# Optimization experiments

Hardware: AMD Instinct MI355X
Metric: run time of the kernel (lower is better)

## Reference

```python
import math
import jax, jax.numpy as jnp
import numpy as np

B, S, H = 2, 2048, 1024
NH = 16
HD = H // NH            # 64
ROT = int(HD * 0.25)    # 16
QKV_SLOTS = 1024
PROJ_SLOTS = 1024
FFN_SLOTS = 4096
EPS = 1e-5


def gelu_l2_norm(x, axis=-1):
    # F.gelu (exact erf) then L2-normalize and rescale by sqrt(dim)
    g = jax.nn.gelu(x, approximate=False)
    n = jnp.linalg.norm(g, ord=2, axis=axis, keepdims=True)
    return g / n * math.sqrt(g.shape[axis])


def layer_norm(x, w, b):
    mu = jnp.mean(x, axis=-1, keepdims=True)
    var = jnp.mean(jnp.square(x - mu), axis=-1, keepdims=True)
    return (x - mu) * jax.lax.rsqrt(var + EPS) * w + b


def pattention(x, key_tok, val_tok):
    # [.., in] @ [slots, in]^T -> [.., slots]; NOTE: scale MULTIPLIES (as in source)
    aw = jnp.einsum('bsh,ph->bsp', x, key_tok) * math.sqrt(x.shape[-1])
    aw = gelu_l2_norm(aw, axis=-1)
    return jnp.einsum('bsp,pd->bsd', aw, val_tok)


def rotary_cos_sin(seq_len, rot_dim, base=10000.0):
    inv_freq = 1.0 / (base ** (jnp.arange(0, rot_dim, 2, dtype=jnp.float32) / rot_dim))
    t = jnp.arange(seq_len, dtype=jnp.float32)
    freqs = jnp.einsum('s,d->sd', t, inv_freq)           # [S, rot/2]
    emb = jnp.concatenate([freqs, freqs], axis=-1)       # [S, rot]
    return jnp.cos(emb), jnp.sin(emb)


def rotate_half(x):
    x1, x2 = jnp.split(x, 2, axis=-1)
    return jnp.concatenate([-x2, x1], axis=-1)


def setup_inputs() -> dict:
    key = jax.random.key(0)
    ks = jax.random.split(key, 12)
    p = lambda k, shape: jax.random.normal(k, shape, dtype=jnp.float32) * 0.02
    return {
        'x': jax.random.normal(ks[0], (B, S, H), dtype=jnp.float32),
        'ln1_w': jnp.ones((H,), jnp.float32), 'ln1_b': jnp.zeros((H,), jnp.float32),
        'ln2_w': jnp.ones((H,), jnp.float32), 'ln2_b': jnp.zeros((H,), jnp.float32),
        'q_key': p(ks[1], (QKV_SLOTS, H)), 'q_val': p(ks[2], (QKV_SLOTS, H)),
        'k_key': p(ks[3], (QKV_SLOTS, H)), 'k_val': p(ks[4], (QKV_SLOTS, H)),
        'v_key': p(ks[5], (QKV_SLOTS, H)), 'v_val': p(ks[6], (QKV_SLOTS, H)),
        'proj_key': p(ks[7], (PROJ_SLOTS, H)), 'proj_val': p(ks[8], (PROJ_SLOTS, H)),
        'ffn_key': p(ks[9], (FFN_SLOTS, H)), 'ffn_val': p(ks[10], (FFN_SLOTS, H)),
    }


def reference(x, ln1_w, ln1_b, ln2_w, ln2_b, q_key, q_val, k_key, k_val,
              v_key, v_val, proj_key, proj_val, ffn_key, ffn_val):
    residual = x
    xn = layer_norm(x, ln1_w, ln1_b)
    q = pattention(xn, q_key, q_val).reshape(B, S, NH, HD)
    k = pattention(xn, k_key, k_val).reshape(B, S, NH, HD)
    v = pattention(xn, v_key, v_val).reshape(B, S, NH, HD)

    cos, sin = rotary_cos_sin(S, ROT)          # [S, ROT]
    cos = cos[None, :, None, :]
    sin = sin[None, :, None, :]
    q_rot, q_pass = q[..., :ROT], q[..., ROT:]
    k_rot, k_pass = k[..., :ROT], k[..., ROT:]
    q_rot = q_rot * cos + rotate_half(q_rot) * sin
    k_rot = k_rot * cos + rotate_half(k_rot) * sin
    q = jnp.concatenate([q_rot, q_pass], axis=-1).transpose(0, 2, 1, 3)  # [B,NH,S,HD]
    k = jnp.concatenate([k_rot, k_pass], axis=-1).transpose(0, 2, 1, 3)
    v = v.transpose(0, 2, 1, 3)

    scale = math.sqrt(HD)
    causal = jnp.triu(jnp.ones((S, S), dtype=bool), k=1)
    attn_mask = jnp.where(causal, jnp.float32(-10000.0), jnp.float32(0.0))
    aw = jnp.einsum('bhqd,bhkd->bhqk', q, k) / scale + attn_mask
    aw = gelu_l2_norm(aw, axis=-1)
    o = jnp.einsum('bhqk,bhkd->bhqd', aw, v)
    o = o.transpose(0, 2, 1, 3).reshape(B, S, H)

    x = residual + pattention(o, proj_key, proj_val)
    residual = x
    x = residual + pattention(layer_norm(x, ln2_w, ln2_b), ffn_key, ffn_val)
    return x
```

## Files before the change

### kernel.cpp

```cpp
#include <hip/hip_runtime.h>

typedef __bf16 bf16x8 __attribute__((ext_vector_type(8)));
typedef float f32x4 __attribute__((ext_vector_type(4)));
typedef unsigned short u16;

__device__ __forceinline__ float b2f(u16 u) {
  union { unsigned int i; float f; } v; v.i = ((unsigned int)u) << 16; return v.f;
}
__device__ __forceinline__ u16 f2b(float f) {
  union { float f; unsigned int i; } v; v.f = f;
  unsigned int x = v.i;
  x += 0x7fffu + ((x >> 16) & 1u);
  return (u16)(x >> 16);
}
__device__ __forceinline__ float gelu_f(float x) {
  float x2 = x * x;
  float p = x * (1.5957691216f + 0.0713548162f * x2);
  float e = __expf(p);
  float r = __builtin_amdgcn_rcpf(1.0f + e);
  return x - x * r;
}
__device__ __forceinline__ void async16(const u16* g, u16* l) {
  __builtin_amdgcn_global_load_lds(
      (const __attribute__((address_space(1))) void*)g,
      (__attribute__((address_space(3))) void*)l, 16, 0, 0);
}
__device__ __forceinline__ void swz(int& bn, int& bm, int& bz) {
  int gx = (int)gridDim.x, gy = (int)gridDim.y;
  int flat = (int)(blockIdx.x + gridDim.x * (blockIdx.y + gridDim.y * blockIdx.z));
  int seq = flat >> 3;
  int nbm = gy >> 3;
  bm = (flat & 7) * nbm + seq % nbm;
  int rest = seq / nbm;
  bn = rest % gx;
  bz = rest / gx;
}

union U4 { uint4 u; u16 s[8]; };
union PF { bf16x8 v; u16 s[8]; };

__global__ __launch_bounds__(256) void cvt9_kernel(
    const float* __restrict__ qk, const float* __restrict__ kk,
    const float* __restrict__ vk, const float* __restrict__ pk,
    const float* __restrict__ fk, u16* __restrict__ w, float* __restrict__ ssqz) {
  int z = blockIdx.y;
  int i = blockIdx.x * 256 + threadIdx.x;
  if (z == 8) {
    if (i < 20480) ssqz[i] = 0.f;
    return;
  }
  const float* in = (z == 0) ? qk : (z == 1) ? kk : (z == 2) ? vk : (z == 3) ? pk
                    : fk + (size_t)(z - 4) * 1048576;
  u16* o = w + (size_t)z * 1048576;
  float4 f = ((const float4*)in)[i];
  ushort4 s;
  s.x = f2b(f.x); s.y = f2b(f.y); s.z = f2b(f.z); s.w = f2b(f.w);
  ((ushort4*)o)[i] = s;
}

__global__ __launch_bounds__(256) void cvtT8_kernel(
    const float* __restrict__ qv, const float* __restrict__ kv,
    const float* __restrict__ vv, const float* __restrict__ pv,
    const float* __restrict__ fv, u16* __restrict__ valsT, u16* __restrict__ fvT) {
  __shared__ float t[32][33];
  int z = blockIdx.z;
  const float* in; u16* o; int Rout, rowoff;
  if (z < 4) {
    in = (z == 0) ? qv : (z == 1) ? kv : (z == 2) ? vv : pv;
    o = valsT + (size_t)z * 1048576; Rout = 1024; rowoff = 0;
  } else {
    in = fv + (size_t)(z - 4) * 1048576;
    o = fvT; Rout = 4096; rowoff = (z - 4) * 1024;
  }
  int bc = blockIdx.x, br = blockIdx.y;
  int tid = threadIdx.x;
  int r = tid >> 5, cc = tid & 31;
  #pragma unroll
  for (int i = 0; i < 4; ++i)
    t[r + i * 8][cc] = in[(size_t)(br * 32 + r + i * 8) * 1024 + bc * 32 + cc];
  __syncthreads();
  #pragma unroll
  for (int i = 0; i < 4; ++i)
    o[(size_t)(bc * 32 + r + i * 8) * Rout + rowoff + br * 32 + cc] = f2b(t[cc][r + i * 8]);
}

__global__ __launch_bounds__(256) void ln_kernel(const float* __restrict__ x,
    const float* __restrict__ w, const float* __restrict__ b, u16* __restrict__ out) {
  int wv = threadIdx.x >> 6, lane = threadIdx.x & 63;
  int row = blockIdx.x * 4 + wv;
  const float* xr = x + (size_t)row * 1024;
  float4 v[4];
  float s = 0.f, s2 = 0.f;
  #pragma unroll
  for (int i = 0; i < 4; ++i) {
    v[i] = ((const float4*)xr)[lane + 64 * i];
    s += v[i].x + v[i].y + v[i].z + v[i].w;
    s2 += v[i].x * v[i].x + v[i].y * v[i].y + v[i].z * v[i].z + v[i].w * v[i].w;
  }
  #pragma unroll
  for (int m = 1; m < 64; m <<= 1) { s += __shfl_xor(s, m); s2 += __shfl_xor(s2, m); }
  float mu = s * (1.0f / 1024.0f);
  float inv = rsqrtf(s2 * (1.0f / 1024.0f) - mu * mu + 1e-5f);
  u16* orow = out + (size_t)row * 1024;
  #pragma unroll
  for (int i = 0; i < 4; ++i) {
    int c = (lane + 64 * i) * 4;
    ushort4 o;
    o.x = f2b((v[i].x - mu) * inv * w[c]     + b[c]);
    o.y = f2b((v[i].y - mu) * inv * w[c + 1] + b[c + 1]);
    o.z = f2b((v[i].z - mu) * inv * w[c + 2] + b[c + 2]);
    o.w = f2b((v[i].w - mu) * inv * w[c + 3] + b[c + 3]);
    ((ushort4*)orow)[lane + 64 * i] = o;
  }
}

__device__ __forceinline__ bf16x8 ldfrag(const u16* __restrict__ base, int row, int ks, int quad) {
  int off = (row * 64 + ks * 32 + quad * 8) ^ ((row & 7) << 3);
  return *(const bf16x8*)&base[off];
}

template <int EPI, bool ROT>
__global__ __launch_bounds__(512, 2) void gemm8(
    const u16* __restrict__ A, size_t sAz,
    const u16* __restrict__ B, size_t sBz,
    u16* __restrict__ C, size_t sCz,
    float* __restrict__ ssqb, size_t sSz,
    int N, int K, float alpha) {
  __shared__ __align__(16) u16 As[2][2][8192];
  __shared__ __align__(16) u16 Bs[2][2][8192];
  int bn, bm, bz;
  swz(bn, bm, bz);
  int tid = threadIdx.x, lane = tid & 63, wv = tid >> 6;
  int quad = lane >> 4, l16 = lane & 15;
  int wm = wv >> 2, wn = wv & 3;
  const u16* Ab = A + (size_t)bz * sAz + (size_t)(bm * 256) * K;
  const u16* Bb = B + (size_t)bz * sBz + (size_t)(bn * 256) * K;
  size_t off0, off1;
  {
    int r0 = wv * 16 + (lane >> 3);
    int r1 = r0 + 8;
    off0 = (size_t)r0 * K + ((lane & 7) ^ (r0 & 7)) * 8;
    off1 = (size_t)r1 * K + ((lane & 7) ^ (r1 & 7)) * 8;
  }
  int lds0 = wv * 1024, lds1 = wv * 1024 + 512;
  const size_t hK = (size_t)128 * K;
  auto STAGE = [&](const u16* gb, int k0, u16* lds) {
    async16(gb + off0 + k0, lds + lds0);
    async16(gb + off1 + k0, lds + lds1);
  };

  f32x4 zero = {0.f, 0.f, 0.f, 0.f};
  f32x4 acc[8][4];
  #pragma unroll
  for (int i = 0; i < 8; ++i)
    #pragma unroll
    for (int j = 0; j < 4; ++j) acc[i][j] = zero;

  int NT = K >> 6;
  STAGE(Bb,      0, &Bs[0][0][0]);
  STAGE(Bb + hK, 0, &Bs[0][1][0]);
  STAGE(Ab,      0, &As[0][0][0]);
  STAGE(Ab + hK, 0, &As[0][1][0]);
  STAGE(Bb,      64, &Bs[1][0][0]);
  STAGE(Bb + hK, 64, &Bs[1][1][0]);
  STAGE(Ab,      64, &As[1][0][0]);
  asm volatile("s_waitcnt vmcnt(6)" ::: "memory");
  __builtin_amdgcn_sched_barrier(0);
  __builtin_amdgcn_s_barrier();

  bf16x8 a[4][2], b[4][2];
  int brow = (wn & 1) * 64;
  for (int t = 0; t < NT; ++t) {
    int cur = t & 1;
    const u16* Ar = &As[cur][wm][0];
    const u16* Br = &Bs[cur][wn >> 1][0];
    #pragma unroll
    for (int j = 0; j < 4; ++j)
      #pragma unroll
      for (int ks = 0; ks < 2; ++ks)
        b[j][ks] = ldfrag(Br, brow + j * 16 + l16, ks, quad);
    #pragma unroll
    for (int i = 0; i < 4; ++i)
      #pragma unroll
      for (int ks = 0; ks < 2; ++ks)
        a[i][ks] = ldfrag(Ar, i * 16 + l16, ks, quad);
    if (t + 1 < NT) STAGE(Ab + hK, (t + 1) * 64, &As[cur ^ 1][1][0]);
    __builtin_amdgcn_s_barrier();
    asm volatile("s_waitcnt lgkmcnt(0)" ::: "memory");
    __builtin_amdgcn_sched_barrier(0);
    __builtin_amdgcn_s_setprio(1);
    #pragma unroll
    for (int i = 0; i < 4; ++i)
      #pragma unroll
      for (int j = 0; j < 2; ++j) {
        acc[i][j] = __builtin_amdgcn_mfma_f32_16x16x32_bf16(a[i][0], b[j][0], acc[i][j], 0, 0, 0);
        acc[i][j] = __builtin_amdgcn_mfma_f32_16x16x32_bf16(a[i][1], b[j][1], acc[i][j], 0, 0, 0);
      }
    __builtin_amdgcn_s_setprio(0);
    __builtin_amdgcn_sched_barrier(0);
    __builtin_amdgcn_s_barrier();
    if (t + 2 < NT) STAGE(Bb, (t + 2) * 64, &Bs[cur][0][0]);
    __builtin_amdgcn_s_barrier();
    __builtin_amdgcn_s_setprio(1);
    #pragma unroll
    for (int i = 0; i < 4; ++i)
      #pragma unroll
      for (int j = 2; j < 4; ++j) {
        acc[i][j] = __builtin_amdgcn_mfma_f32_16x16x32_bf16(a[i][0], b[j][0], acc[i][j], 0, 0, 0);
        acc[i][j] = __builtin_amdgcn_mfma_f32_16x16x32_bf16(a[i][1], b[j][1], acc[i][j], 0, 0, 0);
      }
    __builtin_amdgcn_s_setprio(0);
    __builtin_amdgcn_sched_barrier(0);
    __builtin_amdgcn_s_barrier();
    #pragma unroll
    for (int i = 0; i < 4; ++i)
      #pragma unroll
      for (int ks = 0; ks < 2; ++ks)
        a[i][ks] = ldfrag(Ar, 64 + i * 16 + l16, ks, quad);
    if (t + 2 < NT) STAGE(Bb + hK, (t + 2) * 64, &Bs[cur][1][0]);
    __builtin_amdgcn_s_barrier();
    asm volatile("s_waitcnt lgkmcnt(0)" ::: "memory");
    __builtin_amdgcn_sched_barrier(0);
    __builtin_amdgcn_s_setprio(1);
    #pragma unroll
    for (int i = 0; i < 4; ++i)
      #pragma unroll
      for (int j = 0; j < 2; ++j) {
        acc[4 + i][j] = __builtin_amdgcn_mfma_f32_16x16x32_bf16(a[i][0], b[j][0], acc[4 + i][j], 0, 0, 0);
        acc[4 + i][j] = __builtin_amdgcn_mfma_f32_16x16x32_bf16(a[i][1], b[j][1], acc[4 + i][j], 0, 0, 0);
      }
    __builtin_amdgcn_s_setprio(0);
    __builtin_amdgcn_sched_barrier(0);
    __builtin_amdgcn_s_barrier();
    if (t + 2 < NT) STAGE(Ab, (t + 2) * 64, &As[cur][0][0]);
    __builtin_amdgcn_s_barrier();
    __builtin_amdgcn_s_setprio(1);
    #pragma unroll
    for (int i = 0; i < 4; ++i)
      #pragma unroll
      for (int j = 2; j < 4; ++j) {
        acc[4 + i][j] = __builtin_amdgcn_mfma_f32_16x16x32_bf16(a[i][0], b[j][0], acc[4 + i][j], 0, 0, 0);
        acc[4 + i][j] = __builtin_amdgcn_mfma_f32_16x16x32_bf16(a[i][1], b[j][1], acc[4 + i][j], 0, 0, 0);
      }
    __builtin_amdgcn_s_setprio(0);
    if (t < NT - 1) {
      if (t == NT - 2) asm volatile("s_waitcnt vmcnt(0)" ::: "memory");
      else             asm volatile("s_waitcnt vmcnt(6)" ::: "memory");
    }
    __builtin_amdgcn_sched_barrier(0);
    __builtin_amdgcn_s_barrier();
  }

  #pragma unroll
  for (int i = 0; i < 8; ++i) {
    int rbase = bm * 256 + wm * 128 + i * 16 + quad * 4;
    if (EPI == 0) {
      float srow[4] = {0.f, 0.f, 0.f, 0.f};
      #pragma unroll
      for (int j = 0; j < 4; ++j) {
        int c = bn * 256 + wn * 64 + j * 16 + l16;
        #pragma unroll
        for (int reg = 0; reg < 4; ++reg) {
          float g = gelu_f(acc[i][j][reg] * alpha);
          srow[reg] += g * g;
          C[(size_t)bz * sCz + (size_t)(rbase + reg) * N + c] = f2b(g);
        }
      }
      #pragma unroll
      for (int reg = 0; reg < 4; ++reg) {
        float s = srow[reg];
        s += __shfl_xor(s, 1); s += __shfl_xor(s, 2);
        s += __shfl_xor(s, 4); s += __shfl_xor(s, 8);
        if (l16 == 0) atomicAdd(&ssqb[bz * sSz + rbase + reg], s);
      }
    } else {
      float sc[4];
      #pragma unroll
      for (int reg = 0; reg < 4; ++reg)
        sc[reg] = alpha * rsqrtf(ssqb[bz * sSz + rbase + reg]);
      #pragma unroll
      for (int j = 0; j < 4; ++j) {
        int c = bn * 256 + wn * 64 + j * 16 + l16;
        #pragma unroll
        for (int reg = 0; reg < 4; ++reg) {
          float vs = acc[i][j][reg] * sc[reg];
          if (ROT && j == 0) {
            float prt = __shfl_xor(vs, 8);
            if (bz < 2) {
              int seq = (rbase + reg) & 2047;
              float fr = exp2f((float)(l16 & 7) * -1.66096404744368f);
              float ang = (float)seq * fr;
              float c_ = __cosf(ang), s_ = __sinf(ang);
              vs = (l16 < 8) ? (vs * c_ - prt * s_) : (vs * c_ + prt * s_);
            }
          }
          C[(size_t)bz * sCz + (size_t)(rbase + reg) * N + c] = f2b(vs);
        }
      }
    }
  }
}

template <int TM>
__global__ __launch_bounds__(256) void gemm_key(
    const u16* __restrict__ A, size_t sAz,
    const u16* __restrict__ B, size_t sBz,
    u16* __restrict__ C, size_t sCz,
    float* __restrict__ ssqb, size_t sSz,
    int N, int K, float alpha) {
  constexpr int AI = TM / 32;
  __shared__ __align__(16) u16 As[2][TM * 32];
  __shared__ __align__(16) u16 Bs[2][128 * 32];
  int bn, bm, bz;
  swz(bn, bm, bz);
  const u16* Ab = A + (size_t)bz * sAz + (size_t)bm * TM * K;
  const u16* Bb = B + (size_t)bz * sBz + (size_t)bn * 128 * K;
  int tid = threadIdx.x, lane = tid & 63, wv = tid >> 6;
  int quad = lane >> 4, l16 = lane & 15;
  int lr = lane >> 2, lc = (lane & 3) * 8;
  int wm = wv >> 1, wn = wv & 1;
  int RB = wm * (TM / 2), CB = wn * 64;
  f32x4 zero = {0.f, 0.f, 0.f, 0.f};
  f32x4 acc[AI][4];
  #pragma unroll
  for (int i = 0; i < AI; ++i)
    #pragma unroll
    for (int j = 0; j < 4; ++j) acc[i][j] = zero;
  #pragma unroll
  for (int t = 0; t < TM / 64; ++t) {
    int ia = wv * (TM / 64) + t;
    async16(Ab + (size_t)(ia * 16 + lr) * K + lc, &As[0][ia * 512]);
  }
  #pragma unroll
  for (int t = 0; t < 2; ++t) {
    int ib = wv * 2 + t;
    async16(Bb + (size_t)(ib * 16 + lr) * K + lc, &Bs[0][ib * 512]);
  }
  for (int k0 = 0, cur = 0; k0 < K; k0 += 32, cur ^= 1) {
    __syncthreads();
    if (k0 + 32 < K) {
      #pragma unroll
      for (int t = 0; t < TM / 64; ++t) {
        int ia = wv * (TM / 64) + t;
        async16(Ab + (size_t)(ia * 16 + lr) * K + k0 + 32 + lc, &As[cur ^ 1][ia * 512]);
      }
      #pragma unroll
      for (int t = 0; t < 2; ++t) {
        int ib = wv * 2 + t;
        async16(Bb + (size_t)(ib * 16 + lr) * K + k0 + 32 + lc, &Bs[cur ^ 1][ib * 512]);
      }
    }
    bf16x8 af[AI], bf[4];
    #pragma unroll
    for (int i = 0; i < AI; ++i)
      af[i] = *(const bf16x8*)&As[cur][(RB + i * 16 + l16) * 32 + quad * 8];
    #pragma unroll
    for (int j = 0; j < 4; ++j)
      bf[j] = *(const bf16x8*)&Bs[cur][(CB + j * 16 + l16) * 32 + quad * 8];
    #pragma unroll
    for (int i = 0; i < AI; ++i)
      #pragma unroll
      for (int j = 0; j < 4; ++j)
        acc[i][j] = __builtin_amdgcn_mfma_f32_16x16x32_bf16(af[i], bf[j], acc[i][j], 0, 0, 0);
  }
  #pragma unroll
  for (int i = 0; i < AI; ++i) {
    int rbase = bm * TM + RB + i * 16 + quad * 4;
    float srow[4] = {0.f, 0.f, 0.f, 0.f};
    #pragma unroll
    for (int j = 0; j < 4; ++j) {
      int c = bn * 128 + CB + j * 16 + l16;
      #pragma unroll
      for (int reg = 0; reg < 4; ++reg) {
        float g = gelu_f(acc[i][j][reg] * alpha);
        srow[reg] += g * g;
        C[(size_t)bz * sCz + (size_t)(rbase + reg) * N + c] = f2b(g);
      }
    }
    #pragma unroll
    for (int reg = 0; reg < 4; ++reg) {
      float s = srow[reg];
      s += __shfl_xor(s, 1); s += __shfl_xor(s, 2);
      s += __shfl_xor(s, 4); s += __shfl_xor(s, 8);
      if (l16 == 0) atomicAdd(&ssqb[bz * sSz + rbase + reg], s);
    }
  }
}

template <int TM, int MODE, bool ROT>
__global__ __launch_bounds__(256) void gemm_val(
    const u16* __restrict__ A, size_t sAz,
    const u16* __restrict__ B, size_t sBz,
    void* __restrict__ C, size_t sCz,
    const float* __restrict__ ssqb, size_t sSz,
    int N, int K, int kzs, int klen, float sqrtP, const float* __restrict__ res) {
  constexpr int AI = TM / 32;
  __shared__ __align__(16) u16 As[2][TM * 32];
  __shared__ __align__(16) u16 Bs[2][128 * 32];
  int bn, bm, bz;
  swz(bn, bm, bz);
  const u16* Ab = A + (size_t)bz * sAz + (size_t)bm * TM * K;
  const u16* Bb = B + (size_t)bz * sBz + (size_t)bn * 128 * K;
  int tid = threadIdx.x, lane = tid & 63, wv = tid >> 6;
  int quad = lane >> 4, l16 = lane & 15;
  int lr = lane >> 2, lc = (lane & 3) * 8;
  int wm = wv >> 1, wn = wv & 1;
  int RB = wm * (TM / 2), CB = wn * 64;
  f32x4 zero = {0.f, 0.f, 0.f, 0.f};
  f32x4 acc[AI][4];
  #pragma unroll
  for (int i = 0; i < AI; ++i)
    #pragma unroll
    for (int j = 0; j < 4; ++j) acc[i][j] = zero;
  int kb0 = bz * kzs;
  #pragma unroll
  for (int t = 0; t < TM / 64; ++t) {
    int ia = wv * (TM / 64) + t;
    async16(Ab + (size_t)(ia * 16 + lr) * K + kb0 + lc, &As[0][ia * 512]);
  }
  #pragma unroll
  for (int t = 0; t < 2; ++t) {
    int ib = wv * 2 + t;
    async16(Bb + (size_t)(ib * 16 + lr) * K + kb0 + lc, &Bs[0][ib * 512]);
  }
  for (int k0 = kb0, cur = 0; k0 < kb0 + klen; k0 += 32, cur ^= 1) {
    __syncthreads();
    if (k0 + 32 < kb0 + klen) {
      #pragma unroll
      for (int t = 0; t < TM / 64; ++t) {
        int ia = wv * (TM / 64) + t;
        async16(Ab + (size_t)(ia * 16 + lr) * K + k0 + 32 + lc, &As[cur ^ 1][ia * 512]);
      }
      #pragma unroll
      for (int t = 0; t < 2; ++t) {
        int ib = wv * 2 + t;
        async16(Bb + (size_t)(ib * 16 + lr) * K + k0 + 32 + lc, &Bs[cur ^ 1][ib * 512]);
      }
    }
    bf16x8 af[AI], bf[4];
    #pragma unroll
    for (int i = 0; i < AI; ++i)
      af[i] = *(const bf16x8*)&As[cur][(RB + i * 16 + l16) * 32 + quad * 8];
    #pragma unroll
    for (int j = 0; j < 4; ++j)
      bf[j] = *(const bf16x8*)&Bs[cur][(CB + j * 16 + l16) * 32 + quad * 8];
    #pragma unroll
    for (int i = 0; i < AI; ++i)
      #pragma unroll
      for (int j = 0; j < 4; ++j)
        acc[i][j] = __builtin_amdgcn_mfma_f32_16x16x32_bf16(af[i], bf[j], acc[i][j], 0, 0, 0);
  }
  #pragma unroll
  for (int i = 0; i < AI; ++i) {
    int rbase = bm * TM + RB + i * 16 + quad * 4;
    float sc[4];
    if (MODE < 2) {
      #pragma unroll
      for (int reg = 0; reg < 4; ++reg)
        sc[reg] = sqrtP * rsqrtf(ssqb[bz * sSz + rbase + reg]);
    }
    #pragma unroll
    for (int j = 0; j < 4; ++j) {
      int c = bn * 128 + CB + j * 16 + l16;
      #pragma unroll
      for (int reg = 0; reg < 4; ++reg) {
        float v = acc[i][j][reg];
        size_t idx = (size_t)(rbase + reg) * N + c;
        if (MODE == 0) {
          float vs = v * sc[reg];
          if (ROT && j == 0) {
            float prt = __shfl_xor(vs, 8);
            if (bz < 2) {
              int seq = (rbase + reg) & 2047;
              float fr = exp2f((float)(l16 & 7) * -1.66096404744368f);
              float ang = (float)seq * fr;
              float c_ = __cosf(ang), s_ = __sinf(ang);
              vs = (l16 < 8) ? (vs * c_ - prt * s_) : (vs * c_ + prt * s_);
            }
          }
          ((u16*)C)[(size_t)bz * sCz + idx] = f2b(vs);
        } else if (MODE == 1) {
          ((float*)C)[idx] = v * sc[reg] + res[idx];
        } else {
          ((float*)C)[(size_t)bz * sCz + idx] = v;
        }
      }
    }
  }
}

__global__ __launch_bounds__(256) void vt_kernel(const u16* __restrict__ vb,
                                                 u16* __restrict__ vT) {
  __shared__ __align__(16) u16 T[64][72];
  int st = blockIdx.x, bh = blockIdx.y;
  int b = bh >> 4, h = bh & 15;
  int tid = threadIdx.x;
  #pragma unroll
  for (int i = 0; i < 2; ++i) {
    int l = tid + 256 * i;
    int s = l >> 3, dc = l & 7;
    *(uint4*)&T[s][dc * 8] =
        *(const uint4*)(vb + (size_t)(b * 2048 + st * 64 + s) * 1024 + h * 64 + dc * 8);
  }
  __syncthreads();
  #pragma unroll
  for (int i = 0; i < 2; ++i) {
    int l = tid + 256 * i;
    int d = l >> 3, scid = l & 7;
    int blk = (scid >> 2) * 32;
    int qq = (scid & 3) * 4;
    U4 u;
    #pragma unroll
    for (int j = 0; j < 8; ++j)
      u.s[j] = T[blk + (j >> 2) * 16 + qq + (j & 3)][d];
    *(uint4*)(vT + ((size_t)bh * 64 + d) * 2048 + st * 64 + scid * 8) = u.u;
  }
}

__global__ __launch_bounds__(256) void attn_kernel(
    const u16* __restrict__ qb, const u16* __restrict__ kb,
    const u16* __restrict__ vT, u16* __restrict__ ob) {
  __shared__ __align__(16) u16 Qs[64 * 64];
  __shared__ __align__(16) u16 Ks[2][64 * 64];
  __shared__ __align__(16) u16 Vts[2][64 * 64];
  int bh = blockIdx.x;
  int qt = 31 - (int)blockIdx.y;
  int b = bh >> 4, h = bh & 15;
  const u16* qp = qb + (size_t)b * 2048 * 1024 + h * 64;
  const u16* kp = kb + (size_t)b * 2048 * 1024 + h * 64;
  const u16* vp = vT + (size_t)bh * 64 * 2048;
  int tid = threadIdx.x, lane = tid & 63, wv = tid >> 6;
  int quad = lane >> 4, l16 = lane & 15;
  int lr8 = lane >> 3, lc8 = (lane & 7) * 8;
  int MR = wv * 16;
  int nkt = qt + 1;
  #pragma unroll
  for (int t = 0; t < 2; ++t) {
    int idx = wv * 2 + t;
    async16(qp + (size_t)(qt * 64 + idx * 8 + lr8) * 1024 + lc8, &Qs[idx * 512]);
    async16(kp + (size_t)(idx * 8 + lr8) * 1024 + lc8, &Ks[0][idx * 512]);
    async16(vp + (size_t)(idx * 8 + lr8) * 2048 + lc8, &Vts[0][idx * 512]);
  }
  f32x4 zero = {0.f, 0.f, 0.f, 0.f};
  f32x4 oacc[4];
  #pragma unroll
  for (int dn = 0; dn < 4; ++dn) oacc[dn] = zero;
  float ssql = 0.f;
  bf16x8 bq0 = {}, bq1 = {};
  for (int kt = 0, cur = 0; kt < nkt; ++kt, cur ^= 1) {
    __syncthreads();
    if (kt == 0) {
      bq0 = *(const bf16x8*)&Qs[(MR + l16) * 64 + quad * 8];
      bq1 = *(const bf16x8*)&Qs[(MR + l16) * 64 + 32 + quad * 8];
    }
    if (kt + 1 < nkt) {
      #pragma unroll
      for (int t = 0; t < 2; ++t) {
        int idx = wv * 2 + t;
        async16(kp + (size_t)((kt + 1) * 64 + idx * 8 + lr8) * 1024 + lc8, &Ks[cur ^ 1][idx * 512]);
        async16(vp + (size_t)(idx * 8 + lr8) * 2048 + (kt + 1) * 64 + lc8, &Vts[cur ^ 1][idx * 512]);
      }
    }
    bool dg = (kt == qt);
    #pragma unroll
    for (int kc = 0; kc < 2; ++kc) {
      PF pf;
      #pragma unroll
      for (int snh = 0; snh < 2; ++snh) {
        int sn = kc * 2 + snh;
        bf16x8 ak0 = *(const bf16x8*)&Ks[cur][(sn * 16 + l16) * 64 + quad * 8];
        bf16x8 ak1 = *(const bf16x8*)&Ks[cur][(sn * 16 + l16) * 64 + 32 + quad * 8];
        f32x4 st = zero;
        st = __builtin_amdgcn_mfma_f32_16x16x32_bf16(ak0, bq0, st, 0, 0, 0);
        st = __builtin_amdgcn_mfma_f32_16x16x32_bf16(ak1, bq1, st, 0, 0, 0);
        #pragma unroll
        for (int r = 0; r < 4; ++r) {
          float gl = gelu_f(st[r] * 0.125f);
          if (dg && (sn * 16 + quad * 4 + r > MR + l16)) gl = 0.f;
          ssql += gl * gl;
          pf.s[snh * 4 + r] = f2b(gl);
        }
      }
      #pragma unroll
      for (int dn = 0; dn < 4; ++dn) {
        bf16x8 bv = *(const bf16x8*)&Vts[cur][(dn * 16 + l16) * 64 + kc * 32 + quad * 8];
        oacc[dn] = __builtin_amdgcn_mfma_f32_16x16x32_bf16(pf.v, bv, oacc[dn], 0, 0, 0);
      }
    }
  }
  ssql += __shfl_xor(ssql, 16);
  ssql += __shfl_xor(ssql, 32);
  float sc = 45.254834f * rsqrtf(ssql);
  #pragma unroll
  for (int dn = 0; dn < 4; ++dn)
    #pragma unroll
    for (int r = 0; r < 4; ++r) {
      float scr = __shfl(sc, quad * 4 + r);
      int row = qt * 64 + MR + quad * 4 + r;
      int col = h * 64 + dn * 16 + l16;
      ob[(size_t)(b * 2048 + row) * 1024 + col] = f2b(oacc[dn][r] * scr);
    }
}

__global__ __launch_bounds__(256) void fin_kernel(
    const float* __restrict__ p0, const float* __restrict__ p1,
    const float* __restrict__ x1, const float* __restrict__ ssqf,
    float* __restrict__ out) {
  int row = blockIdx.x, t = threadIdx.x;
  float s = 64.0f * rsqrtf(ssqf[row]);
  size_t base = (size_t)row * 1024 + t * 4;
  float4 a = *(const float4*)(p0 + base);
  float4 b = *(const float4*)(p1 + base);
  float4 r = *(const float4*)(x1 + base);
  float4 o;
  o.x = r.x + s * (a.x + b.x); o.y = r.y + s * (a.y + b.y);
  o.z = r.z + s * (a.z + b.z); o.w = r.w + s * (a.w + b.w);
  *(float4*)(out + base) = o;
}

extern "C" void kernel_launch(void* const* d_in, const int* in_sizes, int n_in,
                              void* d_out, int out_size, void* d_ws, size_t ws_size,
                              hipStream_t stream) {
  const float* x    = (const float*)d_in[0];
  const float* ln1w = (const float*)d_in[1];
  const float* ln1b = (const float*)d_in[2];
  const float* ln2w = (const float*)d_in[3];
  const float* ln2b = (const float*)d_in[4];
  const float* qk   = (const float*)d_in[5];
  const float* qv   = (const float*)d_in[6];
  const float* kk   = (const float*)d_in[7];
  const float* kv   = (const float*)d_in[8];
  const float* vk   = (const float*)d_in[9];
  const float* vv   = (const float*)d_in[10];
  const float* pk   = (const float*)d_in[11];
  const float* pv   = (const float*)d_in[12];
  const float* fk   = (const float*)d_in[13];
  const float* fv   = (const float*)d_in[14];
  float* out = (float*)d_out;

  const size_t M1 = 1048576;
  u16* w = (u16*)d_ws;
  u16* wkeys  = w;
  u16* wpk    = w + 3 * M1;
  u16* wfk    = w + 4 * M1;
  u16* wvalsT = w + 8 * M1;
  u16* wpvT   = w + 11 * M1;
  u16* wfvT   = w + 12 * M1;
  u16* xn     = w + 16 * M1;
  u16* gq     = w + 20 * M1;
  u16* ob     = w + 20 * M1;
  u16* vT     = w + 24 * M1;
  u16* gp     = w + 28 * M1;
  u16* gf     = w + 20 * M1;
  u16* qb     = w + 36 * M1;
  u16* kb     = w + 40 * M1;
  u16* vb     = w + 44 * M1;
  float* ssq_qkv  = (float*)(w + 48 * M1);
  float* ssq_proj = ssq_qkv + 12288;
  float* ssq_ffn  = ssq_qkv + 16384;
  float* x1 = (float*)(w + 52 * M1);
  float* p0 = (float*)w;
  float* p1 = (float*)(w + 36 * M1);

  dim3 blk(256);
  cvt9_kernel<<<dim3(1024, 9), blk, 0, stream>>>(qk, kk, vk, pk, fk, w, ssq_qkv);
  cvtT8_kernel<<<dim3(32, 32, 8), blk, 0, stream>>>(qv, kv, vv, pv, fv, wvalsT, wfvT);

  ln_kernel<<<1024, blk, 0, stream>>>(x, ln1w, ln1b, xn);
  gemm8<0, false><<<dim3(4, 16, 3), 512, 0, stream>>>(
      xn, 0, wkeys, M1, gq, 4 * M1, ssq_qkv, 4096, 1024, 1024, 32.0f);
  gemm8<1, true><<<dim3(4, 16, 3), 512, 0, stream>>>(
      gq, 4 * M1, wvalsT, M1, qb, 4 * M1, ssq_qkv, 4096, 1024, 1024, 32.0f);

  vt_kernel<<<dim3(32, 32), blk, 0, stream>>>(vb, vT);
  attn_kernel<<<dim3(32, 32), blk, 0, stream>>>(qb, kb, vT, ob);

  gemm_key<64><<<dim3(8, 64, 1), blk, 0, stream>>>(
      ob, 0, wpk, 0, gp, 0, ssq_proj, 0, 1024, 1024, 32.0f);
  gemm_val<64, 1, false><<<dim3(8, 64, 1), blk, 0, stream>>>(
      gp, 0, wpvT, 0, x1, 0, ssq_proj, 0, 1024, 1024, 0, 1024, 32.0f, x);

  ln_kernel<<<1024, blk, 0, stream>>>(x1, ln2w, ln2b, xn);
  gemm8<0, false><<<dim3(16, 16, 1), 512, 0, stream>>>(
      xn, 0, wfk, 0, gf, 0, ssq_ffn, 0, 4096, 1024, 32.0f);
  gemm_val<128, 2, false><<<dim3(8, 32, 2), blk, 0, stream>>>(
      gf, 0, wfvT, 0, p0, 18 * M1, ssq_ffn, 0, 1024, 4096, 2048, 2048, 0.0f, nullptr);
  fin_kernel<<<4096, blk, 0, stream>>>(p0, p1, x1, ssq_ffn, out);
}
```

Measured before the change: 444.1 us.

## Use split-K gemm8 with atomic fp32 epilogue for FFN value GEMM; swizzle attention LDS

Gives gemm8 a K-offset/length split and a new fp32 atomicAdd epilogue, and uses it in place of gemm_val for the FFN value projection (4-way split-K into two partial buffers zeroed by a new kernel). The attention kernel now XOR-swizzles its Q/K/V LDS layout to avoid bank conflicts and converts to bf16 through native casts. The rotary branch is also removed from gemm_val's MODE 0 epilogue. Atomics add contention and an extra zeroing pass in exchange for the faster MFMA pipeline on the largest GEMM.

Result: slower. 476.6 us (+7.3%).

```diff
diff --git a/kernel.cpp b/kernel.cpp
--- a/kernel.cpp
+++ b/kernel.cpp
@@ -37,7 +37,6 @@
 }
 
 union U4 { uint4 u; u16 s[8]; };
-union PF { bf16x8 v; u16 s[8]; };
 
 __global__ __launch_bounds__(256) void cvt9_kernel(
     const float* __restrict__ qk, const float* __restrict__ kk,
@@ -125,7 +124,7 @@
     const u16* __restrict__ B, size_t sBz,
     u16* __restrict__ C, size_t sCz,
     float* __restrict__ ssqb, size_t sSz,
-    int N, int K, float alpha) {
+    int N, int K, int kzs, int klen, float alpha) {
   __shared__ __align__(16) u16 As[2][2][8192];
   __shared__ __align__(16) u16 Bs[2][2][8192];
   int bn, bm, bz;
@@ -135,6 +134,7 @@
   int wm = wv >> 2, wn = wv & 3;
   const u16* Ab = A + (size_t)bz * sAz + (size_t)(bm * 256) * K;
   const u16* Bb = B + (size_t)bz * sBz + (size_t)(bn * 256) * K;
+  int koff = bz * kzs;
   size_t off0, off1;
   {
     int r0 = wv * 16 + (lane >> 3);
@@ -156,14 +156,14 @@
     #pragma unroll
     for (int j = 0; j < 4; ++j) acc[i][j] = zero;
 
-  int NT = K >> 6;
-  STAGE(Bb,      0, &Bs[0][0][0]);
-  STAGE(Bb + hK, 0, &Bs[0][1][0]);
-  STAGE(Ab,      0, &As[0][0][0]);
-  STAGE(Ab + hK, 0, &As[0][1][0]);
-  STAGE(Bb,      64, &Bs[1][0][0]);
-  STAGE(Bb + hK, 64, &Bs[1][1][0]);
-  STAGE(Ab,      64, &As[1][0][0]);
+  int NT = klen >> 6;
+  STAGE(Bb,      koff,      &Bs[0][0][0]);
+  STAGE(Bb + hK, koff,      &Bs[0][1][0]);
+  STAGE(Ab,      koff,      &As[0][0][0]);
+  STAGE(Ab + hK, koff,      &As[0][1][0]);
+  STAGE(Bb,      koff + 64, &Bs[1][0][0]);
+  STAGE(Bb + hK, koff + 64, &Bs[1][1][0]);
+  STAGE(Ab,      koff + 64, &As[1][0][0]);
   asm volatile("s_waitcnt vmcnt(6)" ::: "memory");
   __builtin_amdgcn_sched_barrier(0);
   __builtin_amdgcn_s_barrier();
@@ -184,7 +184,7 @@
       #pragma unroll
       for (int ks = 0; ks < 2; ++ks)
         a[i][ks] = ldfrag(Ar, i * 16 + l16, ks, quad);
-    if (t + 1 < NT) STAGE(Ab + hK, (t + 1) * 64, &As[cur ^ 1][1][0]);
+    if (t + 1 < NT) STAGE(Ab + hK, koff + (t + 1) * 64, &As[cur ^ 1][1][0]);
     __builtin_amdgcn_s_barrier();
     asm volatile("s_waitcnt lgkmcnt(0)" ::: "memory");
     __builtin_amdgcn_sched_barrier(0);
@@ -199,7 +199,7 @@
     __builtin_amdgcn_s_setprio(0);
     __builtin_amdgcn_sched_barrier(0);
     __builtin_amdgcn_s_barrier();
-    if (t + 2 < NT) STAGE(Bb, (t + 2) * 64, &Bs[cur][0][0]);
+    if (t + 2 < NT) STAGE(Bb, koff + (t + 2) * 64, &Bs[cur][0][0]);
     __builtin_amdgcn_s_barrier();
     __builtin_amdgcn_s_setprio(1);
     #pragma unroll
@@ -217,7 +217,7 @@
       #pragma unroll
       for (int ks = 0; ks < 2; ++ks)
         a[i][ks] = ldfrag(Ar, 64 + i * 16 + l16, ks, quad);
-    if (t + 2 < NT) STAGE(Bb + hK, (t + 2) * 64, &Bs[cur][1][0]);
+    if (t + 2 < NT) STAGE(Bb + hK, koff + (t + 2) * 64, &Bs[cur][1][0]);
     __builtin_amdgcn_s_barrier();
     asm volatile("s_waitcnt lgkmcnt(0)" ::: "memory");
     __builtin_amdgcn_sched_barrier(0);
@@ -232,7 +232,7 @@
     __builtin_amdgcn_s_setprio(0);
     __builtin_amdgcn_sched_barrier(0);
     __builtin_amdgcn_s_barrier();
-    if (t + 2 < NT) STAGE(Ab, (t + 2) * 64, &As[cur][0][0]);
+    if (t + 2 < NT) STAGE(Ab, koff + (t + 2) * 64, &As[cur][0][0]);
     __builtin_amdgcn_s_barrier();
     __builtin_amdgcn_s_setprio(1);
     #pragma unroll
@@ -273,7 +273,7 @@
         s += __shfl_xor(s, 4); s += __shfl_xor(s, 8);
         if (l16 == 0) atomicAdd(&ssqb[bz * sSz + rbase + reg], s);
       }
-    } else {
+    } else if (EPI == 1) {
       float sc[4];
       #pragma unroll
       for (int reg = 0; reg < 4; ++reg)
@@ -297,8 +297,25 @@
           C[(size_t)bz * sCz + (size_t)(rbase + reg) * N + c] = f2b(vs);
         }
       }
-    }
-  }
+    } else {
+      float* Cf = (float*)C + (size_t)(bz >> 1) * sCz;
+      #pragma unroll
+      for (int j = 0; j < 4; ++j) {
+        int c = bn * 256 + wn * 64 + j * 16 + l16;
+        #pragma unroll
+        for (int reg = 0; reg < 4; ++reg)
+          atomicAdd(&Cf[(size_t)(rbase + reg) * N + c], acc[i][j][reg]);
+      }
+    }
+  }
+}
+
+__global__ __launch_bounds__(256) void zz_kernel(float* __restrict__ p0,
+                                                 float* __restrict__ p1) {
+  size_t i = ((size_t)blockIdx.x * 256 + threadIdx.x) * 4;
+  float4 z = {0.f, 0.f, 0.f, 0.f};
+  *(float4*)(p0 + i) = z;
+  *(float4*)(p1 + i) = z;
 }
 
 template <int TM>
@@ -467,18 +484,7 @@
         float v = acc[i][j][reg];
         size_t idx = (size_t)(rbase + reg) * N + c;
         if (MODE == 0) {
-          float vs = v * sc[reg];
-          if (ROT && j == 0) {
-            float prt = __shfl_xor(vs, 8);
-            if (bz < 2) {
-              int seq = (rbase + reg) & 2047;
-              float fr = exp2f((float)(l16 & 7) * -1.66096404744368f);
-              float ang = (float)seq * fr;
-              float c_ = __cosf(ang), s_ = __sinf(ang);
-              vs = (l16 < 8) ? (vs * c_ - prt * s_) : (vs * c_ + prt * s_);
-            }
-          }
-          ((u16*)C)[(size_t)bz * sCz + idx] = f2b(vs);
+          ((u16*)C)[(size_t)bz * sCz + idx] = f2b(v * sc[reg]);
         } else if (MODE == 1) {
           ((float*)C)[idx] = v * sc[reg] + res[idx];
         } else {
@@ -531,15 +537,17 @@
   const u16* vp = vT + (size_t)bh * 64 * 2048;
   int tid = threadIdx.x, lane = tid & 63, wv = tid >> 6;
   int quad = lane >> 4, l16 = lane & 15;
-  int lr8 = lane >> 3, lc8 = (lane & 7) * 8;
+  int lr8 = lane >> 3;
+  int lc8s = ((lane & 7) ^ lr8) * 8;
+  int rx = (l16 & 7) << 3;
   int MR = wv * 16;
   int nkt = qt + 1;
   #pragma unroll
   for (int t = 0; t < 2; ++t) {
     int idx = wv * 2 + t;
-    async16(qp + (size_t)(qt * 64 + idx * 8 + lr8) * 1024 + lc8, &Qs[idx * 512]);
-    async16(kp + (size_t)(idx * 8 + lr8) * 1024 + lc8, &Ks[0][idx * 512]);
-    async16(vp + (size_t)(idx * 8 + lr8) * 2048 + lc8, &Vts[0][idx * 512]);
+    async16(qp + (size_t)(qt * 64 + idx * 8 + lr8) * 1024 + lc8s, &Qs[idx * 512]);
+    async16(kp + (size_t)(idx * 8 + lr8) * 1024 + lc8s, &Ks[0][idx * 512]);
+    async16(vp + (size_t)(idx * 8 + lr8) * 2048 + lc8s, &Vts[0][idx * 512]);
   }
   f32x4 zero = {0.f, 0.f, 0.f, 0.f};
   f32x4 oacc[4];
@@ -550,26 +558,26 @@
   for (int kt = 0, cur = 0; kt < nkt; ++kt, cur ^= 1) {
     __syncthreads();
     if (kt == 0) {
-      bq0 = *(const bf16x8*)&Qs[(MR + l16) * 64 + quad * 8];
-      bq1 = *(const bf16x8*)&Qs[(MR + l16) * 64 + 32 + quad * 8];
+      bq0 = *(const bf16x8*)&Qs[((MR + l16) * 64 + quad * 8) ^ rx];
+      bq1 = *(const bf16x8*)&Qs[((MR + l16) * 64 + 32 + quad * 8) ^ rx];
     }
     if (kt + 1 < nkt) {
       #pragma unroll
       for (int t = 0; t < 2; ++t) {
         int idx = wv * 2 + t;
-        async16(kp + (size_t)((kt + 1) * 64 + idx * 8 + lr8) * 1024 + lc8, &Ks[cur ^ 1][idx * 512]);
-        async16(vp + (size_t)(idx * 8 + lr8) * 2048 + (kt + 1) * 64 + lc8, &Vts[cur ^ 1][idx * 512]);
+        async16(kp + (size_t)((kt + 1) * 64 + idx * 8 + lr8) * 1024 + lc8s, &Ks[cur ^ 1][idx * 512]);
+        async16(vp + (size_t)(idx * 8 + lr8) * 2048 + (kt + 1) * 64 + lc8s, &Vts[cur ^ 1][idx * 512]);
       }
     }
     bool dg = (kt == qt);
     #pragma unroll
     for (int kc = 0; kc < 2; ++kc) {
-      PF pf;
+      bf16x8 pf;
       #pragma unroll
       for (int snh = 0; snh < 2; ++snh) {
         int sn = kc * 2 + snh;
-        bf16x8 ak0 = *(const bf16x8*)&Ks[cur][(sn * 16 + l16) * 64 + quad * 8];
-        bf16x8 ak1 = *(const bf16x8*)&Ks[cur][(sn * 16 + l16) * 64 + 32 + quad * 8];
+        bf16x8 ak0 = *(const bf16x8*)&Ks[cur][((sn * 16 + l16) * 64 + quad * 8) ^ rx];
+        bf16x8 ak1 = *(const bf16x8*)&Ks[cur][((sn * 16 + l16) * 64 + 32 + quad * 8) ^ rx];
         f32x4 st = zero;
         st = __builtin_amdgcn_mfma_f32_16x16x32_bf16(ak0, bq0, st, 0, 0, 0);
         st = __builtin_amdgcn_mfma_f32_16x16x32_bf16(ak1, bq1, st, 0, 0, 0);
@@ -578,13 +586,13 @@
           float gl = gelu_f(st[r] * 0.125f);
           if (dg && (sn * 16 + quad * 4 + r > MR + l16)) gl = 0.f;
           ssql += gl * gl;
-          pf.s[snh * 4 + r] = f2b(gl);
+          pf[snh * 4 + r] = (__bf16)gl;
         }
       }
       #pragma unroll
       for (int dn = 0; dn < 4; ++dn) {
-        bf16x8 bv = *(const bf16x8*)&Vts[cur][(dn * 16 + l16) * 64 + kc * 32 + quad * 8];
-        oacc[dn] = __builtin_amdgcn_mfma_f32_16x16x32_bf16(pf.v, bv, oacc[dn], 0, 0, 0);
+        bf16x8 bv = *(const bf16x8*)&Vts[cur][((dn * 16 + l16) * 64 + kc * 32 + quad * 8) ^ rx];
+        oacc[dn] = __builtin_amdgcn_mfma_f32_16x16x32_bf16(pf, bv, oacc[dn], 0, 0, 0);
       }
     }
   }
@@ -668,9 +676,9 @@
 
   ln_kernel<<<1024, blk, 0, stream>>>(x, ln1w, ln1b, xn);
   gemm8<0, false><<<dim3(4, 16, 3), 512, 0, stream>>>(
-      xn, 0, wkeys, M1, gq, 4 * M1, ssq_qkv, 4096, 1024, 1024, 32.0f);
+      xn, 0, wkeys, M1, gq, 4 * M1, ssq_qkv, 4096, 1024, 1024, 0, 1024, 32.0f);
   gemm8<1, true><<<dim3(4, 16, 3), 512, 0, stream>>>(
-      gq, 4 * M1, wvalsT, M1, qb, 4 * M1, ssq_qkv, 4096, 1024, 1024, 32.0f);
+      gq, 4 * M1, wvalsT, M1, qb, 4 * M1, ssq_qkv, 4096, 1024, 1024, 0, 1024, 32.0f);
 
   vt_kernel<<<dim3(32, 32), blk, 0, stream>>>(vb, vT);
   attn_kernel<<<dim3(32, 32), blk, 0, stream>>>(qb, kb, vT, ob);
@@ -682,8 +690,9 @@
 
   ln_kernel<<<1024, blk, 0, stream>>>(x1, ln2w, ln2b, xn);
   gemm8<0, false><<<dim3(16, 16, 1), 512, 0, stream>>>(
-      xn, 0, wfk, 0, gf, 0, ssq_ffn, 0, 4096, 1024, 32.0f);
-  gemm_val<128, 2, false><<<dim3(8, 32, 2), blk, 0, stream>>>(
-      gf, 0, wfvT, 0, p0, 18 * M1, ssq_ffn, 0, 1024, 4096, 2048, 2048, 0.0f, nullptr);
+      xn, 0, wfk, 0, gf, 0, ssq_ffn, 0, 4096, 1024, 0, 1024, 32.0f);
+  zz_kernel<<<4096, blk, 0, stream>>>(p0, p1);
+  gemm8<2, false><<<dim3(4, 16, 4), 512, 0, stream>>>(
+      gf, 0, wfvT, 0, (u16*)p0, 18 * M1, ssq_ffn, 0, 1024, 4096, 1024, 1024, 0.0f);
   fin_kernel<<<4096, blk, 0, stream>>>(p0, p1, x1, ssq_ffn, out);
 }
```
